# Kernel tuning notes

Measured on AMD Instinct MI355X. Metric: run time of the kernel, lower is better.

The kernel has to match this reference:

```python
import jax, jax.numpy as jnp
import numpy as np

NEG_SLOPE = 0.2

def gat_conv(x_s, x_d, src, dst, W_s, W_d, a_s, a_d, bias, n_dst):
    # PyG GATConv, heads=1, bipartite (-1,-1) input
    hs = x_s @ W_s                          # [Ns, H]
    hd = x_d @ W_d                          # [Nd, H]
    e = jnp.take(hs @ a_s, src) + jnp.take(hd @ a_d, dst)   # [E]
    e = jax.nn.leaky_relu(e, NEG_SLOPE)
    emax = jax.ops.segment_max(e, dst, num_segments=n_dst)
    emax = jax.lax.stop_gradient(jnp.where(jnp.isfinite(emax), emax, 0.0))
    w = jnp.exp(e - emax[dst])              # [E]
    den = jax.ops.segment_sum(w, dst, num_segments=n_dst)   # [Nd]
    msg = jax.ops.segment_sum(w[:, None] * hs[src], dst, num_segments=n_dst)  # [Nd, H]
    return msg / jnp.maximum(den, 1e-16)[:, None] + bias

def setup_inputs() -> dict:
    key = jax.random.key(0)
    ks = jax.random.split(key, 16)
    Na, Nw, D, H, E = 50000, 100000, 128, 128, 640000
    s = 1.0 / np.sqrt(D)
    return {
        "x_artist": jax.random.normal(ks[0], (Na, D), jnp.float32),
        "x_artwork": jax.random.normal(ks[1], (Nw, D), jnp.float32),
        "src_ca": jax.random.randint(ks[2], (E,), 0, Na, jnp.int32),
        "dst_ca": jax.random.randint(ks[3], (E,), 0, Nw, jnp.int32),
        "src_ac": jax.random.randint(ks[4], (E,), 0, Nw, jnp.int32),
        "dst_ac": jax.random.randint(ks[5], (E,), 0, Na, jnp.int32),
        "src_ww": jax.random.randint(ks[6], (E,), 0, Nw, jnp.int32),
        "dst_ww": jax.random.randint(ks[7], (E,), 0, Nw, jnp.int32),
        "Ws": jax.random.normal(ks[8], (3, D, H), jnp.float32) * s,
        "Wd": jax.random.normal(ks[9], (3, D, H), jnp.float32) * s,
        "a_s": jax.random.normal(ks[10], (3, H), jnp.float32) * s,
        "a_d": jax.random.normal(ks[11], (3, H), jnp.float32) * s,
        "b": jax.random.normal(ks[12], (3, H), jnp.float32) * 0.01,
    }

def reference(x_artist, x_artwork, src_ca, dst_ca, src_ac, dst_ac, src_ww, dst_ww, Ws, Wd, a_s, a_d, b):
    Na, Nw = x_artist.shape[0], x_artwork.shape[0]
    # edge type 0: artist->artwork (creates); 1: artwork->artist; 2: artwork->artwork
    out_aw = gat_conv(x_artist, x_artwork, src_ca, dst_ca, Ws[0], Wd[0], a_s[0], a_d[0], b[0], Nw)
    out_aw = out_aw + gat_conv(x_artwork, x_artwork, src_ww, dst_ww, Ws[2], Wd[2], a_s[2], a_d[2], b[2], Nw)  # HeteroConv aggr='sum'
    out_ar = gat_conv(x_artwork, x_artist, src_ac, dst_ac, Ws[1], Wd[1], a_s[1], a_d[1], b[1], Na)
    out_ar = jax.nn.relu(out_ar)
    out_aw = jax.nn.relu(out_aw)
    # concat node-type outputs: [Na+Nw, H]
    return jnp.concatenate([out_ar, out_aw], axis=0)
```

## Files before the change

kernel.cpp:

```cpp
#include <hip/hip_runtime.h>
#include <hip/hip_bf16.h>

#define HD 128
#define NEG_SLOPE 0.2f

typedef __attribute__((ext_vector_type(8))) short short8;
typedef __attribute__((ext_vector_type(4))) float f32x4;

__device__ __forceinline__ float lrelu(float x) {
    return x > 0.f ? x : NEG_SLOPE * x;
}
__device__ __forceinline__ ushort f2bf(float f) {
    __hip_bfloat16 h = __float2bfloat16(f);
    return *(ushort*)&h;
}
__device__ __forceinline__ float bflo(unsigned u) { return __uint_as_float(u << 16); }
__device__ __forceinline__ float bfhi(unsigned u) { return __uint_as_float(u & 0xffff0000u); }

__global__ void k_prep(const float* __restrict__ Ws, const float* __restrict__ Wd,
                       const float* __restrict__ a_s, const float* __restrict__ a_d,
                       ushort* __restrict__ Wt, ushort* __restrict__ vfA,
                       ushort* __restrict__ vfW, int* __restrict__ counts, int nTot) {
    int t = blockIdx.x * blockDim.x + threadIdx.x;
    if (t < nTot) counts[t] = 0;
    if (t < 768) {
        int c = t >> 8;
        int sd = (t >> 7) & 1;
        int d = t & (HD - 1);
        const float* W = sd ? Wd : Ws;
        const float* a = sd ? a_d : a_s;
        const float* Wrow = W + ((size_t)c * HD + d) * HD;
        const float* av = a + c * HD;
        float s = 0.f;
        for (int h = 0; h < HD; h++) s += Wrow[h] * av[h];
        ushort bs = f2bf(s);
        if (c == 0 && sd == 0)      vfA[0 * HD + d] = bs;
        else if (c == 1 && sd == 1) vfA[1 * HD + d] = bs;
        else if (c == 0 && sd == 1) vfW[0 * HD + d] = bs;
        else if (c == 1 && sd == 0) vfW[1 * HD + d] = bs;
        else if (c == 2 && sd == 0) vfW[2 * HD + d] = bs;
        else                        vfW[3 * HD + d] = bs;
    }
    int z = t - 768;
    if (z >= 0 && z < 14 * HD) vfA[2 * HD + z] = 0;
    int z2 = t - 768 - 14 * HD;
    if (z2 >= 0 && z2 < 12 * HD) vfW[4 * HD + z2] = 0;
    int u = t - 768 - 14 * HD - 12 * HD;
    if (u >= 0 && u < 3 * HD * HD) {
        int c = u >> 14;
        int r = u & 16383;
        int n = r >> 7, k = r & 127;
        Wt[u] = f2bf(Ws[((size_t)c << 14) + k * HD + n]);
    }
}

template<int NV>
__device__ __forceinline__ void gemm_body(int blk, const float* __restrict__ X,
        const ushort* __restrict__ Wt, const ushort* __restrict__ vfrag,
        ushort* __restrict__ H16,
        float* __restrict__ a0, float* __restrict__ a1,
        float* __restrict__ a2, float* __restrict__ a3, int nrows) {
    int tid = threadIdx.x;
    int lane = tid & 63;
    int wv = tid >> 6;
    int m = lane & 15;
    int kb = lane >> 4;
    long long row0 = (long long)blk * 64 + wv * 16;
    long long ar = row0 + m;
    if (ar >= nrows) ar = nrows - 1;
    const float* aptr = X + ar * HD + kb * 8;
    const ushort* bptr = Wt + (size_t)m * HD + kb * 8;

    f32x4 acc[8];
    #pragma unroll
    for (int t = 0; t < 8; t++) acc[t] = (f32x4){0.f, 0.f, 0.f, 0.f};
    f32x4 aacc = (f32x4){0.f, 0.f, 0.f, 0.f};

    #pragma unroll
    for (int ks = 0; ks < 4; ks++) {
        float4 A0 = *(const float4*)(aptr + ks * 32);
        float4 A1 = *(const float4*)(aptr + ks * 32 + 4);
        short8 af;
        af[0] = (short)f2bf(A0.x); af[1] = (short)f2bf(A0.y);
        af[2] = (short)f2bf(A0.z); af[3] = (short)f2bf(A0.w);
        af[4] = (short)f2bf(A1.x); af[5] = (short)f2bf(A1.y);
        af[6] = (short)f2bf(A1.z); af[7] = (short)f2bf(A1.w);
        #pragma unroll
        for (int t = 0; t < 8; t++) {
            short8 bf = *(const short8*)(bptr + (size_t)t * 16 * HD + ks * 32);
            acc[t] = __builtin_amdgcn_mfma_f32_16x16x32_bf16(af, bf, acc[t], 0, 0, 0);
        }
        if (NV > 0) {
            short8 vf = *(const short8*)(vfrag + (size_t)m * HD + kb * 8 + ks * 32);
            aacc = __builtin_amdgcn_mfma_f32_16x16x32_bf16(af, vf, aacc, 0, 0, 0);
        }
    }
    int rb = kb * 4;
    #pragma unroll
    for (int t = 0; t < 8; t++) {
        #pragma unroll
        for (int j = 0; j < 4; j++) {
            long long r = row0 + rb + j;
            if (r < nrows) H16[r * HD + t * 16 + m] = f2bf(acc[t][j]);
        }
    }
    if (NV > 0 && m < NV) {
        float* ao = (m == 0) ? a0 : (m == 1) ? a1 : (m == 2) ? a2 : a3;
        #pragma unroll
        for (int j = 0; j < 4; j++) {
            long long r = row0 + rb + j;
            if (r < nrows) ao[r] = aacc[j];
        }
    }
}

__global__ __launch_bounds__(256) void k_hist_gemm(
        const int* __restrict__ d0, const int* __restrict__ d1, const int* __restrict__ d2,
        int* __restrict__ counts, ushort* __restrict__ rank16, int E, int off1, int off2,
        const float* __restrict__ xa, int Na, const ushort* __restrict__ Wt0,
        const ushort* __restrict__ vfA, ushort* __restrict__ hs0,
        float* __restrict__ as0, float* __restrict__ ad1, int g0B,
        const float* __restrict__ xw, int Nw, const ushort* __restrict__ Wt2,
        const ushort* __restrict__ vfW, ushort* __restrict__ hs2,
        float* __restrict__ ad0, float* __restrict__ as1,
        float* __restrict__ as2, float* __restrict__ ad2,
        int ngemm, int total) {
    int b = blockIdx.x;
    int g0 = (int)(((long long)b * ngemm) / total);
    int g1 = (int)(((long long)(b + 1) * ngemm) / total);
    if (g1 > g0) {
        if (g0 < g0B)
            gemm_body<2>(g0, xa, Wt0, vfA, hs0, as0, ad1, nullptr, nullptr, Na);
        else
            gemm_body<4>(g0 - g0B, xw, Wt2, vfW, hs2, ad0, as1, as2, ad2, Nw);
    } else {
        int hb = b - g0;
        int t = hb * 256 + threadIdx.x;
        if (t >= 3 * E) return;
        int gd;
        if (t < E)           gd = d0[t];
        else if (t < 2 * E)  gd = off1 + d1[t - E];
        else                 gd = off2 + d2[t - 2 * E];
        rank16[t] = (ushort)atomicAdd(&counts[gd], 1);
    }
}

__global__ __launch_bounds__(256) void k_gemm1(const float* __restrict__ X,
        const ushort* __restrict__ Wt, ushort* __restrict__ H16, int nrows) {
    gemm_body<0>(blockIdx.x, X, Wt, nullptr, H16, nullptr, nullptr, nullptr, nullptr, nrows);
}

__global__ void k_chunksum(const int* __restrict__ counts, int* __restrict__ chunkSum, int n) {
    __shared__ int sh[256];
    int i = blockIdx.x * 256 + threadIdx.x;
    sh[threadIdx.x] = (i < n) ? counts[i] : 0;
    __syncthreads();
    for (int off = 128; off; off >>= 1) {
        if (threadIdx.x < off) sh[threadIdx.x] += sh[threadIdx.x + off];
        __syncthreads();
    }
    if (threadIdx.x == 0) chunkSum[blockIdx.x] = sh[0];
}

__global__ void k_scanchunk(const int* __restrict__ chunkSum, int* __restrict__ chunkOff, int nChunk) {
    __shared__ int sh[1024];
    int t = threadIdx.x;
    int v = (t < nChunk) ? chunkSum[t] : 0;
    sh[t] = v;
    __syncthreads();
    for (int off = 1; off < 1024; off <<= 1) {
        int add = (t >= off) ? sh[t - off] : 0;
        __syncthreads();
        sh[t] += add;
        __syncthreads();
    }
    if (t < nChunk) chunkOff[t] = sh[t] - v;
}

__global__ void k_rowstart(const int* __restrict__ counts, const int* __restrict__ chunkOff,
                           int* __restrict__ rowStart, int n) {
    __shared__ int sh[256];
    int i = blockIdx.x * 256 + threadIdx.x;
    int t = threadIdx.x;
    int v = (i < n) ? counts[i] : 0;
    sh[t] = v;
    __syncthreads();
    for (int off = 1; off < 256; off <<= 1) {
        int add = (t >= off) ? sh[t - off] : 0;
        __syncthreads();
        sh[t] += add;
        __syncthreads();
    }
    if (i < n) rowStart[i] = chunkOff[blockIdx.x] + sh[t] - v;
}

__global__ void k_fill3(const int* __restrict__ s0, const int* __restrict__ d0,
                        const int* __restrict__ s1, const int* __restrict__ d1,
                        const int* __restrict__ s2, const int* __restrict__ d2,
                        const float* __restrict__ as0, const float* __restrict__ as1,
                        const float* __restrict__ as2,
                        const int* __restrict__ rowStart, const ushort* __restrict__ rank16,
                        int2* __restrict__ ePair, int E, int off1, int off2) {
    int t = blockIdx.x * blockDim.x + threadIdx.x;
    if (t >= 3 * E) return;
    int sv, gd;
    const float* A;
    if (t < E)          { sv = s0[t];        gd = d0[t];        A = as0; }
    else if (t < 2 * E) { int e = t - E;     sv = s1[e]; gd = off1 + d1[e]; A = as1; }
    else                { int e = t - 2 * E; sv = s2[e]; gd = off2 + d2[e]; A = as2; }
    ePair[rowStart[gd] + rank16[t]] = make_int2(sv, __float_as_int(A[sv]));
}

__device__ __forceinline__ void seg_accum(int2 p, int dg, int base, float adv,
                                          const int2* __restrict__ ePair,
                                          const ushort* __restrict__ hs,
                                          int lane, int sub, int fl, float acc[8]) {
    if (dg <= 0) return;
    if (dg <= 64) {
        float av = (lane < dg) ? lrelu(__int_as_float(p.y) + adv) : -1e30f;
        float mm = av;
        #pragma unroll
        for (int off = 32; off; off >>= 1) mm = fmaxf(mm, __shfl_xor(mm, off, 64));
        float w = (lane < dg) ? __expf(av - mm) : 0.f;
        float den = w;
        #pragma unroll
        for (int off = 32; off; off >>= 1) den += __shfl_xor(den, off, 64);
        w *= (1.f / den);
        int s = (lane < dg) ? p.x : 0;
        for (int j0 = 0; j0 < dg; j0 += 4) {
            int idx = j0 + sub;
            float wj = __shfl(w, idx, 64);
            int sj = __shfl(s, idx, 64);
            uint4 u = *(const uint4*)((const unsigned*)hs + ((size_t)sj * HD + fl * 8) / 2);
            acc[0] += wj * bflo(u.x); acc[1] += wj * bfhi(u.x);
            acc[2] += wj * bflo(u.y); acc[3] += wj * bfhi(u.y);
            acc[4] += wj * bflo(u.z); acc[5] += wj * bfhi(u.z);
            acc[6] += wj * bflo(u.w); acc[7] += wj * bfhi(u.w);
        }
    } else {
        float mm = -1e30f;
        for (int i = lane; i < dg; i += 64) {
            int2 q = ePair[base + i];
            mm = fmaxf(mm, lrelu(__int_as_float(q.y) + adv));
        }
        #pragma unroll
        for (int off = 32; off; off >>= 1) mm = fmaxf(mm, __shfl_xor(mm, off, 64));
        float den = 0.f;
        for (int i = lane; i < dg; i += 64) {
            int2 q = ePair[base + i];
            den += __expf(lrelu(__int_as_float(q.y) + adv) - mm);
        }
        #pragma unroll
        for (int off = 32; off; off >>= 1) den += __shfl_xor(den, off, 64);
        float inv = 1.f / den;
        for (int c0 = 0; c0 < dg; c0 += 64) {
            int n = min(64, dg - c0);
            int s = 0; float w = 0.f;
            if (lane < n) {
                int2 q = ePair[base + c0 + lane];
                s = q.x;
                w = __expf(lrelu(__int_as_float(q.y) + adv) - mm) * inv;
            }
            for (int j0 = 0; j0 < n; j0 += 4) {
                int idx = j0 + sub;
                float wj = __shfl(w, idx, 64);
                int sj = __shfl(s, idx, 64);
                uint4 u = *(const uint4*)((const unsigned*)hs + ((size_t)sj * HD + fl * 8) / 2);
                acc[0] += wj * bflo(u.x); acc[1] += wj * bfhi(u.x);
                acc[2] += wj * bflo(u.y); acc[3] += wj * bfhi(u.y);
                acc[4] += wj * bflo(u.z); acc[5] += wj * bfhi(u.z);
                acc[6] += wj * bflo(u.w); acc[7] += wj * bfhi(u.w);
            }
        }
    }
}

__global__ __launch_bounds__(256) void k_agg02(const int2* __restrict__ ePair,
        const int* __restrict__ rowStart, const int* __restrict__ counts,
        const float* __restrict__ ad0_, const float* __restrict__ ad2_,
        const ushort* __restrict__ hs0, const ushort* __restrict__ hs2,
        const float* __restrict__ b0, const float* __restrict__ b2,
        float* __restrict__ out, int Nw, int offR2) {
    int lane = threadIdx.x & 63;
    int d = (int)(((long long)blockIdx.x * blockDim.x + threadIdx.x) >> 6);
    if (d >= Nw) return;
    int sub = lane >> 4, fl = lane & 15;

    int dgA = counts[d],         bA = rowStart[d];
    int dgB = counts[offR2 + d], bB = rowStart[offR2 + d];
    float aA = ad0_[d], aB = ad2_[d];
    int2 pA = make_int2(0, 0), pB = make_int2(0, 0);
    if (dgA > 0 && dgA <= 64 && lane < dgA) pA = ePair[bA + lane];
    if (dgB > 0 && dgB <= 64 && lane < dgB) pB = ePair[bB + lane];

    float acc[8];
    #pragma unroll
    for (int k = 0; k < 8; k++) acc[k] = 0.f;
    seg_accum(pA, dgA, bA, aA, ePair, hs0, lane, sub, fl, acc);
    seg_accum(pB, dgB, bB, aB, ePair, hs2, lane, sub, fl, acc);

    #pragma unroll
    for (int k = 0; k < 8; k++) {
        acc[k] += __shfl_xor(acc[k], 16, 64);
        acc[k] += __shfl_xor(acc[k], 32, 64);
    }
    if (lane < 16) {
        float* orow = out + (size_t)d * HD + fl * 8;
        float vals[8];
        #pragma unroll
        for (int k = 0; k < 8; k++)
            vals[k] = fmaxf(b0[fl * 8 + k] + b2[fl * 8 + k] + acc[k], 0.f);
        *(float4*)&orow[0] = make_float4(vals[0], vals[1], vals[2], vals[3]);
        *(float4*)&orow[4] = make_float4(vals[4], vals[5], vals[6], vals[7]);
    }
}

__global__ __launch_bounds__(256) void k_agg1(const int2* __restrict__ ePair,
        const int* __restrict__ rowStart, const int* __restrict__ counts,
        const float* __restrict__ ad_, const ushort* __restrict__ hs,
        const float* __restrict__ bias, float* __restrict__ out, int Nd) {
    int lane = threadIdx.x & 63;
    int w = (int)(((long long)blockIdx.x * blockDim.x + threadIdx.x) >> 6);
    int d0 = 2 * w, d1 = 2 * w + 1;
    if (d0 >= Nd) return;
    int sub = lane >> 4, fl = lane & 15;

    int dg0 = counts[d0], b0 = rowStart[d0];
    float a0 = ad_[d0];
    int dg1 = 0, b1 = 0; float a1 = 0.f;
    if (d1 < Nd) { dg1 = counts[d1]; b1 = rowStart[d1]; a1 = ad_[d1]; }
    int2 p0 = make_int2(0, 0), p1 = make_int2(0, 0);
    if (dg0 > 0 && dg0 <= 64 && lane < dg0) p0 = ePair[b0 + lane];
    if (dg1 > 0 && dg1 <= 64 && lane < dg1) p1 = ePair[b1 + lane];

    float acc0[8], acc1[8];
    #pragma unroll
    for (int k = 0; k < 8; k++) { acc0[k] = 0.f; acc1[k] = 0.f; }
    seg_accum(p0, dg0, b0, a0, ePair, hs, lane, sub, fl, acc0);
    seg_accum(p1, dg1, b1, a1, ePair, hs, lane, sub, fl, acc1);

    #pragma unroll
    for (int k = 0; k < 8; k++) {
        acc0[k] += __shfl_xor(acc0[k], 16, 64);
        acc0[k] += __shfl_xor(acc0[k], 32, 64);
        acc1[k] += __shfl_xor(acc1[k], 16, 64);
        acc1[k] += __shfl_xor(acc1[k], 32, 64);
    }
    if (lane < 16) {
        float* orow = out + (size_t)d0 * HD + fl * 8;
        float vals[8];
        #pragma unroll
        for (int k = 0; k < 8; k++)
            vals[k] = fmaxf(bias[fl * 8 + k] + acc0[k], 0.f);
        *(float4*)&orow[0] = make_float4(vals[0], vals[1], vals[2], vals[3]);
        *(float4*)&orow[4] = make_float4(vals[4], vals[5], vals[6], vals[7]);
        if (d1 < Nd) {
            float* orow1 = out + (size_t)d1 * HD + fl * 8;
            #pragma unroll
            for (int k = 0; k < 8; k++)
                vals[k] = fmaxf(bias[fl * 8 + k] + acc1[k], 0.f);
            *(float4*)&orow1[0] = make_float4(vals[0], vals[1], vals[2], vals[3]);
            *(float4*)&orow1[4] = make_float4(vals[4], vals[5], vals[6], vals[7]);
        }
    }
}

extern "C" void kernel_launch(void* const* d_in, const int* in_sizes, int n_in,
                              void* d_out, int out_size, void* d_ws, size_t ws_size,
                              hipStream_t stream) {
    const float* x_artist  = (const float*)d_in[0];
    const float* x_artwork = (const float*)d_in[1];
    const int* srcA[3] = {(const int*)d_in[2], (const int*)d_in[4], (const int*)d_in[6]};
    const int* dstA[3] = {(const int*)d_in[3], (const int*)d_in[5], (const int*)d_in[7]};
    const float* Ws  = (const float*)d_in[8];
    const float* Wd  = (const float*)d_in[9];
    const float* a_s = (const float*)d_in[10];
    const float* a_d = (const float*)d_in[11];
    const float* b   = (const float*)d_in[12];
    float* out = (float*)d_out;

    const int Na = in_sizes[0] / HD;
    const int Nw = in_sizes[1] / HD;
    const int E  = in_sizes[2];
    const int nTot = Nw + Na + Nw;
    const int nChunk = (nTot + 255) / 256;

    float* ws = (float*)d_ws;
    size_t off = 0;
    float* as0 = ws + off;  off += Na;
    float* ad1 = ws + off;  off += Na;
    float* ad0 = ws + off;  off += Nw;
    float* as1 = ws + off;  off += Nw;
    float* as2 = ws + off;  off += Nw;
    float* ad2 = ws + off;  off += Nw;
    int* counts   = (int*)(ws + off); off += nTot;
    int* chunkSum = (int*)(ws + off); off += 1024;
    int* chunkOff = (int*)(ws + off); off += 1024;
    int* rowStart = (int*)(ws + off); off += nTot;
    int2* ePair   = (int2*)(ws + off); off += (size_t)2 * 3 * E;
    ushort* rank16 = (ushort*)(ws + off); off += ((size_t)3 * E + 1) / 2;
    ushort* Wt    = (ushort*)(ws + off); off += (3 * HD * HD) / 2;
    ushort* vfA   = (ushort*)(ws + off); off += (16 * HD) / 2;
    ushort* vfW   = (ushort*)(ws + off); off += (16 * HD) / 2;
    ushort* hs0   = (ushort*)(ws + off); off += (size_t)Na * HD / 2;
    ushort* hs2   = (ushort*)(ws + off); off += (size_t)Nw * HD / 2;
    if (ws_size < off * sizeof(float) || nChunk > 1024) return;

    const int off1 = Nw, off2 = Nw + Na;
    const int B = 256;

    k_prep<<<(nTot + B - 1) / B, B, 0, stream>>>(Ws, Wd, a_s, a_d, Wt, vfA, vfW, counts, nTot);

    const int histB = (3 * E + B - 1) / B;
    const int g0B = (Na + 63) / 64;
    const int g2B = (Nw + 63) / 64;
    const int ngemm = g0B + g2B;
    const int total = histB + ngemm;
    k_hist_gemm<<<total, B, 0, stream>>>(dstA[0], dstA[1], dstA[2], counts, rank16,
                                         E, off1, off2,
                                         x_artist, Na, Wt + 0 * HD * HD, vfA, hs0,
                                         as0, ad1, g0B,
                                         x_artwork, Nw, Wt + 2 * HD * HD, vfW, hs2,
                                         ad0, as1, as2, ad2,
                                         ngemm, total);

    k_chunksum<<<nChunk, B, 0, stream>>>(counts, chunkSum, nTot);
    k_scanchunk<<<1, 1024, 0, stream>>>(chunkSum, chunkOff, nChunk);
    k_rowstart<<<nChunk, B, 0, stream>>>(counts, chunkOff, rowStart, nTot);

    k_fill3<<<(3 * E + B - 1) / B, B, 0, stream>>>(srcA[0], dstA[0], srcA[1], dstA[1],
                                                   srcA[2], dstA[2], as0, as1, as2,
                                                   rowStart, rank16, ePair, E, off1, off2);

    k_agg02<<<(Nw + 3) / 4, B, 0, stream>>>(ePair, rowStart, counts, ad0, ad2,
                                            hs0, hs2, b, b + 2 * HD,
                                            out + (size_t)Na * HD, Nw, off2);
    k_gemm1<<<(Nw + 63) / 64, B, 0, stream>>>(x_artwork, Wt + 1 * HD * HD, hs2, Nw);
    int nw1 = (Na + 1) / 2;
    k_agg1<<<(nw1 + 3) / 4, B, 0, stream>>>(ePair, rowStart + off1, counts + off1,
                                            ad1, hs2, b + HD, out, Na);
}
```

Measured before the change: 282.7 us.

## Split hist/GEMM fusion, compute both artwork projections in one pass, pipeline gathers

Splits the combined histogram+GEMM kernel into separate histogram and GEMM kernels. When workspace allows, a new kernel computes the artwork projections for edge types 1 and 2 in a single pass over x_artwork, writing into separate buffers, so the later standalone gemm1 launch is skipped. The small-degree gather loop is also software-pipelined so the next row load is issued before the current one is accumulated. This costs extra workspace memory and removes the overlap the fused hist/GEMM launch gave between atomics and GEMM work.

```diff
diff --git a/kernel.cpp b/kernel.cpp
--- a/kernel.cpp
+++ b/kernel.cpp
@@ -60,9 +60,8 @@
         ushort* __restrict__ H16,
         float* __restrict__ a0, float* __restrict__ a1,
         float* __restrict__ a2, float* __restrict__ a3, int nrows) {
-    int tid = threadIdx.x;
-    int lane = tid & 63;
-    int wv = tid >> 6;
+    int lane = threadIdx.x & 63;
+    int wv = threadIdx.x >> 6;
     int m = lane & 15;
     int kb = lane >> 4;
     long long row0 = (long long)blk * 64 + wv * 16;
@@ -114,40 +113,101 @@
     }
 }
 
-__global__ __launch_bounds__(256) void k_hist_gemm(
-        const int* __restrict__ d0, const int* __restrict__ d1, const int* __restrict__ d2,
-        int* __restrict__ counts, ushort* __restrict__ rank16, int E, int off1, int off2,
-        const float* __restrict__ xa, int Na, const ushort* __restrict__ Wt0,
-        const ushort* __restrict__ vfA, ushort* __restrict__ hs0,
-        float* __restrict__ as0, float* __restrict__ ad1, int g0B,
-        const float* __restrict__ xw, int Nw, const ushort* __restrict__ Wt2,
-        const ushort* __restrict__ vfW, ushort* __restrict__ hs2,
-        float* __restrict__ ad0, float* __restrict__ as1,
-        float* __restrict__ as2, float* __restrict__ ad2,
-        int ngemm, int total) {
-    int b = blockIdx.x;
-    int g0 = (int)(((long long)b * ngemm) / total);
-    int g1 = (int)(((long long)(b + 1) * ngemm) / total);
-    if (g1 > g0) {
-        if (g0 < g0B)
-            gemm_body<2>(g0, xa, Wt0, vfA, hs0, as0, ad1, nullptr, nullptr, Na);
-        else
-            gemm_body<4>(g0 - g0B, xw, Wt2, vfW, hs2, ad0, as1, as2, ad2, Nw);
-    } else {
-        int hb = b - g0;
-        int t = hb * 256 + threadIdx.x;
-        if (t >= 3 * E) return;
-        int gd;
-        if (t < E)           gd = d0[t];
-        else if (t < 2 * E)  gd = off1 + d1[t - E];
-        else                 gd = off2 + d2[t - 2 * E];
-        rank16[t] = (ushort)atomicAdd(&counts[gd], 1);
-    }
-}
-
-__global__ __launch_bounds__(256) void k_gemm1(const float* __restrict__ X,
+__global__ __launch_bounds__(256) void k_gemm0(const float* __restrict__ X,
+        const ushort* __restrict__ Wt, const ushort* __restrict__ vfA,
+        ushort* __restrict__ H16, float* __restrict__ as0, float* __restrict__ ad1, int nrows) {
+    gemm_body<2>(blockIdx.x, X, Wt, vfA, H16, as0, ad1, nullptr, nullptr, nrows);
+}
+__global__ __launch_bounds__(256) void k_gemm2f(const float* __restrict__ X,
+        const ushort* __restrict__ Wt, const ushort* __restrict__ vfW,
+        ushort* __restrict__ H16, float* __restrict__ ad0, float* __restrict__ as1,
+        float* __restrict__ as2, float* __restrict__ ad2, int nrows) {
+    gemm_body<4>(blockIdx.x, X, Wt, vfW, H16, ad0, as1, as2, ad2, nrows);
+}
+__global__ __launch_bounds__(256) void k_gemm1f(const float* __restrict__ X,
         const ushort* __restrict__ Wt, ushort* __restrict__ H16, int nrows) {
     gemm_body<0>(blockIdx.x, X, Wt, nullptr, H16, nullptr, nullptr, nullptr, nullptr, nrows);
+}
+
+__global__ __launch_bounds__(256) void k_gemmW(const float* __restrict__ X,
+        const ushort* __restrict__ WtA, const ushort* __restrict__ WtB,
+        const ushort* __restrict__ vf, ushort* __restrict__ hsA, ushort* __restrict__ hsB,
+        float* __restrict__ a0, float* __restrict__ a1,
+        float* __restrict__ a2, float* __restrict__ a3, int nrows) {
+    int lane = threadIdx.x & 63;
+    int wv = threadIdx.x >> 6;
+    int m = lane & 15;
+    int kb = lane >> 4;
+    long long row0 = (long long)blockIdx.x * 64 + wv * 16;
+    long long ar = row0 + m;
+    if (ar >= nrows) ar = nrows - 1;
+    const float* aptr = X + ar * HD + kb * 8;
+    const ushort* bA = WtA + (size_t)m * HD + kb * 8;
+    const ushort* bB = WtB + (size_t)m * HD + kb * 8;
+    int rb = kb * 4;
+
+    #pragma unroll
+    for (int half = 0; half < 2; half++) {
+        f32x4 accA[4], accB[4];
+        #pragma unroll
+        for (int t = 0; t < 4; t++) {
+            accA[t] = (f32x4){0.f, 0.f, 0.f, 0.f};
+            accB[t] = (f32x4){0.f, 0.f, 0.f, 0.f};
+        }
+        f32x4 aacc = (f32x4){0.f, 0.f, 0.f, 0.f};
+        #pragma unroll
+        for (int ks = 0; ks < 4; ks++) {
+            float4 A0 = *(const float4*)(aptr + ks * 32);
+            float4 A1 = *(const float4*)(aptr + ks * 32 + 4);
+            short8 af;
+            af[0] = (short)f2bf(A0.x); af[1] = (short)f2bf(A0.y);
+            af[2] = (short)f2bf(A0.z); af[3] = (short)f2bf(A0.w);
+            af[4] = (short)f2bf(A1.x); af[5] = (short)f2bf(A1.y);
+            af[6] = (short)f2bf(A1.z); af[7] = (short)f2bf(A1.w);
+            #pragma unroll
+            for (int t = 0; t < 4; t++) {
+                short8 bfA = *(const short8*)(bA + (size_t)(half * 4 + t) * 16 * HD + ks * 32);
+                accA[t] = __builtin_amdgcn_mfma_f32_16x16x32_bf16(af, bfA, accA[t], 0, 0, 0);
+                short8 bfB = *(const short8*)(bB + (size_t)(half * 4 + t) * 16 * HD + ks * 32);
+                accB[t] = __builtin_amdgcn_mfma_f32_16x16x32_bf16(af, bfB, accB[t], 0, 0, 0);
+            }
+            if (half == 0) {
+                short8 vfr = *(const short8*)(vf + (size_t)m * HD + kb * 8 + ks * 32);
+                aacc = __builtin_amdgcn_mfma_f32_16x16x32_bf16(af, vfr, aacc, 0, 0, 0);
+            }
+        }
+        #pragma unroll
+        for (int t = 0; t < 4; t++) {
+            #pragma unroll
+            for (int j = 0; j < 4; j++) {
+                long long r = row0 + rb + j;
+                if (r < nrows) {
+                    hsA[r * HD + (half * 4 + t) * 16 + m] = f2bf(accA[t][j]);
+                    hsB[r * HD + (half * 4 + t) * 16 + m] = f2bf(accB[t][j]);
+                }
+            }
+        }
+        if (half == 0 && m < 4) {
+            float* ao = (m == 0) ? a0 : (m == 1) ? a1 : (m == 2) ? a2 : a3;
+            #pragma unroll
+            for (int j = 0; j < 4; j++) {
+                long long r = row0 + rb + j;
+                if (r < nrows) ao[r] = aacc[j];
+            }
+        }
+    }
+}
+
+__global__ void k_hist3(const int* __restrict__ d0, const int* __restrict__ d1,
+                        const int* __restrict__ d2, int* __restrict__ counts,
+                        ushort* __restrict__ rank16, int E, int off1, int off2) {
+    int t = blockIdx.x * blockDim.x + threadIdx.x;
+    if (t >= 3 * E) return;
+    int gd;
+    if (t < E)           gd = d0[t];
+    else if (t < 2 * E)  gd = off1 + d1[t - E];
+    else                 gd = off2 + d2[t - 2 * E];
+    rank16[t] = (ushort)atomicAdd(&counts[gd], 1);
 }
 
 __global__ void k_chunksum(const int* __restrict__ counts, int* __restrict__ chunkSum, int n) {
@@ -211,6 +271,30 @@
     ePair[rowStart[gd] + rank16[t]] = make_int2(sv, __float_as_int(A[sv]));
 }
 
+__device__ __forceinline__ void acc8(uint4 u, float wj, float acc[8]) {
+    acc[0] += wj * bflo(u.x); acc[1] += wj * bfhi(u.x);
+    acc[2] += wj * bflo(u.y); acc[3] += wj * bfhi(u.y);
+    acc[4] += wj * bflo(u.z); acc[5] += wj * bfhi(u.z);
+    acc[6] += wj * bflo(u.w); acc[7] += wj * bfhi(u.w);
+}
+
+__device__ __forceinline__ void seg_gather_pipe(int s, float w, int dg,
+        const ushort* __restrict__ hs, int sub, int fl, float acc[8]) {
+    if (dg <= 0) return;
+    const unsigned* hp = (const unsigned*)hs + fl * 4;
+    float wj = __shfl(w, sub, 64);
+    int sj = __shfl(s, sub, 64);
+    uint4 u = *(const uint4*)(hp + (size_t)sj * (HD / 2));
+    for (int j0 = 4; j0 < dg; j0 += 4) {
+        float wn = __shfl(w, j0 + sub, 64);
+        int sn = __shfl(s, j0 + sub, 64);
+        uint4 un = *(const uint4*)(hp + (size_t)sn * (HD / 2));
+        acc8(u, wj, acc);
+        wj = wn; u = un;
+    }
+    acc8(u, wj, acc);
+}
+
 __device__ __forceinline__ void seg_accum(int2 p, int dg, int base, float adv,
                                           const int2* __restrict__ ePair,
                                           const ushort* __restrict__ hs,
@@ -227,16 +311,7 @@
         for (int off = 32; off; off >>= 1) den += __shfl_xor(den, off, 64);
         w *= (1.f / den);
         int s = (lane < dg) ? p.x : 0;
-        for (int j0 = 0; j0 < dg; j0 += 4) {
-            int idx = j0 + sub;
-            float wj = __shfl(w, idx, 64);
-            int sj = __shfl(s, idx, 64);
-            uint4 u = *(const uint4*)((const unsigned*)hs + ((size_t)sj * HD + fl * 8) / 2);
-            acc[0] += wj * bflo(u.x); acc[1] += wj * bfhi(u.x);
-            acc[2] += wj * bflo(u.y); acc[3] += wj * bfhi(u.y);
-            acc[4] += wj * bflo(u.z); acc[5] += wj * bfhi(u.z);
-            acc[6] += wj * bflo(u.w); acc[7] += wj * bfhi(u.w);
-        }
+        seg_gather_pipe(s, w, dg, hs, sub, fl, acc);
     } else {
         float mm = -1e30f;
         for (int i = lane; i < dg; i += 64) {
@@ -266,10 +341,7 @@
                 float wj = __shfl(w, idx, 64);
                 int sj = __shfl(s, idx, 64);
                 uint4 u = *(const uint4*)((const unsigned*)hs + ((size_t)sj * HD + fl * 8) / 2);
-                acc[0] += wj * bflo(u.x); acc[1] += wj * bfhi(u.x);
-                acc[2] += wj * bflo(u.y); acc[3] += wj * bfhi(u.y);
-                acc[4] += wj * bflo(u.z); acc[5] += wj * bfhi(u.z);
-                acc[6] += wj * bflo(u.w); acc[7] += wj * bfhi(u.w);
+                acc8(u, wj, acc);
             }
         }
     }
@@ -406,28 +478,33 @@
     ushort* hs2   = (ushort*)(ws + off); off += (size_t)Nw * HD / 2;
     if (ws_size < off * sizeof(float) || nChunk > 1024) return;
 
+    size_t offBig = off + (size_t)Nw * HD / 2;
+    bool bigWS = (ws_size >= offBig * sizeof(float));
+    ushort* hs1 = bigWS ? (ushort*)(ws + off) : hs2;
+
     const int off1 = Nw, off2 = Nw + Na;
     const int B = 256;
 
     k_prep<<<(nTot + B - 1) / B, B, 0, stream>>>(Ws, Wd, a_s, a_d, Wt, vfA, vfW, counts, nTot);
 
-    const int histB = (3 * E + B - 1) / B;
-    const int g0B = (Na + 63) / 64;
-    const int g2B = (Nw + 63) / 64;
-    const int ngemm = g0B + g2B;
-    const int total = histB + ngemm;
-    k_hist_gemm<<<total, B, 0, stream>>>(dstA[0], dstA[1], dstA[2], counts, rank16,
-                                         E, off1, off2,
-                                         x_artist, Na, Wt + 0 * HD * HD, vfA, hs0,
-                                         as0, ad1, g0B,
-                                         x_artwork, Nw, Wt + 2 * HD * HD, vfW, hs2,
-                                         ad0, as1, as2, ad2,
-                                         ngemm, total);
+    k_hist3<<<(3 * E + B - 1) / B, B, 0, stream>>>(dstA[0], dstA[1], dstA[2], counts,
+                                                   rank16, E, off1, off2);
 
     k_chunksum<<<nChunk, B, 0, stream>>>(counts, chunkSum, nTot);
     k_scanchunk<<<1, 1024, 0, stream>>>(chunkSum, chunkOff, nChunk);
     k_rowstart<<<nChunk, B, 0, stream>>>(counts, chunkOff, rowStart, nTot);
 
+    k_gemm0<<<(Na + 63) / 64, B, 0, stream>>>(x_artist, Wt + 0 * HD * HD, vfA,
+                                              hs0, as0, ad1, Na);
+    if (bigWS) {
+        k_gemmW<<<(Nw + 63) / 64, B, 0, stream>>>(x_artwork, Wt + 1 * HD * HD,
+                                                  Wt + 2 * HD * HD, vfW, hs1, hs2,
+                                                  ad0, as1, as2, ad2, Nw);
+    } else {
+        k_gemm2f<<<(Nw + 63) / 64, B, 0, stream>>>(x_artwork, Wt + 2 * HD * HD, vfW,
+                                                   hs2, ad0, as1, as2, ad2, Nw);
+    }
+
     k_fill3<<<(3 * E + B - 1) / B, B, 0, stream>>>(srcA[0], dstA[0], srcA[1], dstA[1],
                                                    srcA[2], dstA[2], as0, as1, as2,
                                                    rowStart, rank16, ePair, E, off1, off2);
@@ -435,8 +512,9 @@
     k_agg02<<<(Nw + 3) / 4, B, 0, stream>>>(ePair, rowStart, counts, ad0, ad2,
                                             hs0, hs2, b, b + 2 * HD,
                                             out + (size_t)Na * HD, Nw, off2);
-    k_gemm1<<<(Nw + 63) / 64, B, 0, stream>>>(x_artwork, Wt + 1 * HD * HD, hs2, Nw);
+    if (!bigWS)
+        k_gemm1f<<<(Nw + 63) / 64, B, 0, stream>>>(x_artwork, Wt + 1 * HD * HD, hs2, Nw);
     int nw1 = (Na + 1) / 2;
     k_agg1<<<(nw1 + 3) / 4, B, 0, stream>>>(ePair, rowStart + off1, counts + off1,
-                                            ad1, hs2, b + HD, out, Na);
-}
+                                            ad1, hs1, b + HD, out, Na);
+}
```

Result: slower. 334.8 us (+18.4%).

## Split hist/gemm kernels, merge scan stages, add separate hs1 buffer, pipeline gathers

Applied to the files above, without the earlier changes.

Separates the fused histogram+GEMM kernel into a standalone histogram kernel and a GEMM kernel. The chunk-offset scan is folded into the row-start kernel, with each block summing preceding chunk sums itself, which removes one launch. When workspace allows, the third projection gets its own buffer and is computed before aggregation instead of overwriting hs2 between the two aggregation kernels. The small-degree gather loop is software-pipelined so the next row load is issued before the current one is accumulated. The trade-off is the loss of the overlap between histogram and GEMM work that the fused kernel provided, plus a redundant prefix sum in every row-start block.

```diff
diff --git a/kernel.cpp b/kernel.cpp
--- a/kernel.cpp
+++ b/kernel.cpp
@@ -60,9 +60,8 @@
         ushort* __restrict__ H16,
         float* __restrict__ a0, float* __restrict__ a1,
         float* __restrict__ a2, float* __restrict__ a3, int nrows) {
-    int tid = threadIdx.x;
-    int lane = tid & 63;
-    int wv = tid >> 6;
+    int lane = threadIdx.x & 63;
+    int wv = threadIdx.x >> 6;
     int m = lane & 15;
     int kb = lane >> 4;
     long long row0 = (long long)blk * 64 + wv * 16;
@@ -114,40 +113,36 @@
     }
 }
 
-__global__ __launch_bounds__(256) void k_hist_gemm(
-        const int* __restrict__ d0, const int* __restrict__ d1, const int* __restrict__ d2,
-        int* __restrict__ counts, ushort* __restrict__ rank16, int E, int off1, int off2,
-        const float* __restrict__ xa, int Na, const ushort* __restrict__ Wt0,
+__global__ __launch_bounds__(256) void k_gemm02(
+        const float* __restrict__ xa, const ushort* __restrict__ Wt0,
         const ushort* __restrict__ vfA, ushort* __restrict__ hs0,
-        float* __restrict__ as0, float* __restrict__ ad1, int g0B,
-        const float* __restrict__ xw, int Nw, const ushort* __restrict__ Wt2,
+        float* __restrict__ as0, float* __restrict__ ad1, int Na, int g0B,
+        const float* __restrict__ xw, const ushort* __restrict__ Wt2,
         const ushort* __restrict__ vfW, ushort* __restrict__ hs2,
         float* __restrict__ ad0, float* __restrict__ as1,
-        float* __restrict__ as2, float* __restrict__ ad2,
-        int ngemm, int total) {
+        float* __restrict__ as2, float* __restrict__ ad2, int Nw) {
     int b = blockIdx.x;
-    int g0 = (int)(((long long)b * ngemm) / total);
-    int g1 = (int)(((long long)(b + 1) * ngemm) / total);
-    if (g1 > g0) {
-        if (g0 < g0B)
-            gemm_body<2>(g0, xa, Wt0, vfA, hs0, as0, ad1, nullptr, nullptr, Na);
-        else
-            gemm_body<4>(g0 - g0B, xw, Wt2, vfW, hs2, ad0, as1, as2, ad2, Nw);
-    } else {
-        int hb = b - g0;
-        int t = hb * 256 + threadIdx.x;
-        if (t >= 3 * E) return;
-        int gd;
-        if (t < E)           gd = d0[t];
-        else if (t < 2 * E)  gd = off1 + d1[t - E];
-        else                 gd = off2 + d2[t - 2 * E];
-        rank16[t] = (ushort)atomicAdd(&counts[gd], 1);
-    }
-}
-
-__global__ __launch_bounds__(256) void k_gemm1(const float* __restrict__ X,
+    if (b < g0B)
+        gemm_body<2>(b, xa, Wt0, vfA, hs0, as0, ad1, nullptr, nullptr, Na);
+    else
+        gemm_body<4>(b - g0B, xw, Wt2, vfW, hs2, ad0, as1, as2, ad2, Nw);
+}
+
+__global__ __launch_bounds__(256) void k_gemm1f(const float* __restrict__ X,
         const ushort* __restrict__ Wt, ushort* __restrict__ H16, int nrows) {
     gemm_body<0>(blockIdx.x, X, Wt, nullptr, H16, nullptr, nullptr, nullptr, nullptr, nrows);
+}
+
+__global__ void k_hist3(const int* __restrict__ d0, const int* __restrict__ d1,
+                        const int* __restrict__ d2, int* __restrict__ counts,
+                        ushort* __restrict__ rank16, int E, int off1, int off2) {
+    int t = blockIdx.x * blockDim.x + threadIdx.x;
+    if (t >= 3 * E) return;
+    int gd;
+    if (t < E)           gd = d0[t];
+    else if (t < 2 * E)  gd = off1 + d1[t - E];
+    else                 gd = off2 + d2[t - 2 * E];
+    rank16[t] = (ushort)atomicAdd(&counts[gd], 1);
 }
 
 __global__ void k_chunksum(const int* __restrict__ counts, int* __restrict__ chunkSum, int n) {
@@ -162,26 +157,23 @@
     if (threadIdx.x == 0) chunkSum[blockIdx.x] = sh[0];
 }
 
-__global__ void k_scanchunk(const int* __restrict__ chunkSum, int* __restrict__ chunkOff, int nChunk) {
-    __shared__ int sh[1024];
+__global__ void k_rowstart2(const int* __restrict__ counts, const int* __restrict__ chunkSum,
+                            int* __restrict__ rowStart, int n) {
+    __shared__ int sh[256];
+    __shared__ int chunkOffS;
+    int bid = blockIdx.x;
     int t = threadIdx.x;
-    int v = (t < nChunk) ? chunkSum[t] : 0;
-    sh[t] = v;
+    int psum = 0;
+    for (int i = t; i < bid; i += 256) psum += chunkSum[i];
+    sh[t] = psum;
     __syncthreads();
-    for (int off = 1; off < 1024; off <<= 1) {
-        int add = (t >= off) ? sh[t - off] : 0;
+    for (int off = 128; off; off >>= 1) {
+        if (t < off) sh[t] += sh[t + off];
         __syncthreads();
-        sh[t] += add;
-        __syncthreads();
-    }
-    if (t < nChunk) chunkOff[t] = sh[t] - v;
-}
-
-__global__ void k_rowstart(const int* __restrict__ counts, const int* __restrict__ chunkOff,
-                           int* __restrict__ rowStart, int n) {
-    __shared__ int sh[256];
-    int i = blockIdx.x * 256 + threadIdx.x;
-    int t = threadIdx.x;
+    }
+    if (t == 0) chunkOffS = sh[0];
+    __syncthreads();
+    int i = bid * 256 + t;
     int v = (i < n) ? counts[i] : 0;
     sh[t] = v;
     __syncthreads();
@@ -191,7 +183,7 @@
         sh[t] += add;
         __syncthreads();
     }
-    if (i < n) rowStart[i] = chunkOff[blockIdx.x] + sh[t] - v;
+    if (i < n) rowStart[i] = chunkOffS + sh[t] - v;
 }
 
 __global__ void k_fill3(const int* __restrict__ s0, const int* __restrict__ d0,
@@ -211,6 +203,30 @@
     ePair[rowStart[gd] + rank16[t]] = make_int2(sv, __float_as_int(A[sv]));
 }
 
+__device__ __forceinline__ void acc8(uint4 u, float wj, float acc[8]) {
+    acc[0] += wj * bflo(u.x); acc[1] += wj * bfhi(u.x);
+    acc[2] += wj * bflo(u.y); acc[3] += wj * bfhi(u.y);
+    acc[4] += wj * bflo(u.z); acc[5] += wj * bfhi(u.z);
+    acc[6] += wj * bflo(u.w); acc[7] += wj * bfhi(u.w);
+}
+
+__device__ __forceinline__ void seg_gather_pipe(int s, float w, int dg,
+        const ushort* __restrict__ hs, int sub, int fl, float acc[8]) {
+    if (dg <= 0) return;
+    const unsigned* hp = (const unsigned*)hs + fl * 4;
+    float wj = __shfl(w, sub, 64);
+    int sj = __shfl(s, sub, 64);
+    uint4 u = *(const uint4*)(hp + (size_t)sj * (HD / 2));
+    for (int j0 = 4; j0 < dg; j0 += 4) {
+        float wn = __shfl(w, j0 + sub, 64);
+        int sn = __shfl(s, j0 + sub, 64);
+        uint4 un = *(const uint4*)(hp + (size_t)sn * (HD / 2));
+        acc8(u, wj, acc);
+        wj = wn; u = un;
+    }
+    acc8(u, wj, acc);
+}
+
 __device__ __forceinline__ void seg_accum(int2 p, int dg, int base, float adv,
                                           const int2* __restrict__ ePair,
                                           const ushort* __restrict__ hs,
@@ -227,16 +243,7 @@
         for (int off = 32; off; off >>= 1) den += __shfl_xor(den, off, 64);
         w *= (1.f / den);
         int s = (lane < dg) ? p.x : 0;
-        for (int j0 = 0; j0 < dg; j0 += 4) {
-            int idx = j0 + sub;
-            float wj = __shfl(w, idx, 64);
-            int sj = __shfl(s, idx, 64);
-            uint4 u = *(const uint4*)((const unsigned*)hs + ((size_t)sj * HD + fl * 8) / 2);
-            acc[0] += wj * bflo(u.x); acc[1] += wj * bfhi(u.x);
-            acc[2] += wj * bflo(u.y); acc[3] += wj * bfhi(u.y);
-            acc[4] += wj * bflo(u.z); acc[5] += wj * bfhi(u.z);
-            acc[6] += wj * bflo(u.w); acc[7] += wj * bfhi(u.w);
-        }
+        seg_gather_pipe(s, w, dg, hs, sub, fl, acc);
     } else {
         float mm = -1e30f;
         for (int i = lane; i < dg; i += 64) {
@@ -266,10 +273,7 @@
                 float wj = __shfl(w, idx, 64);
                 int sj = __shfl(s, idx, 64);
                 uint4 u = *(const uint4*)((const unsigned*)hs + ((size_t)sj * HD + fl * 8) / 2);
-                acc[0] += wj * bflo(u.x); acc[1] += wj * bfhi(u.x);
-                acc[2] += wj * bflo(u.y); acc[3] += wj * bfhi(u.y);
-                acc[4] += wj * bflo(u.z); acc[5] += wj * bfhi(u.z);
-                acc[6] += wj * bflo(u.w); acc[7] += wj * bfhi(u.w);
+                acc8(u, wj, acc);
             }
         }
     }
@@ -394,8 +398,7 @@
     float* as2 = ws + off;  off += Nw;
     float* ad2 = ws + off;  off += Nw;
     int* counts   = (int*)(ws + off); off += nTot;
-    int* chunkSum = (int*)(ws + off); off += 1024;
-    int* chunkOff = (int*)(ws + off); off += 1024;
+    int* chunkSum = (int*)(ws + off); off += nChunk;
     int* rowStart = (int*)(ws + off); off += nTot;
     int2* ePair   = (int2*)(ws + off); off += (size_t)2 * 3 * E;
     ushort* rank16 = (ushort*)(ws + off); off += ((size_t)3 * E + 1) / 2;
@@ -404,29 +407,31 @@
     ushort* vfW   = (ushort*)(ws + off); off += (16 * HD) / 2;
     ushort* hs0   = (ushort*)(ws + off); off += (size_t)Na * HD / 2;
     ushort* hs2   = (ushort*)(ws + off); off += (size_t)Nw * HD / 2;
-    if (ws_size < off * sizeof(float) || nChunk > 1024) return;
+    if (ws_size < off * sizeof(float)) return;
+
+    size_t offBig = off + (size_t)Nw * HD / 2;
+    bool bigWS = (ws_size >= offBig * sizeof(float));
+    ushort* hs1 = bigWS ? (ushort*)(ws + off) : hs2;
 
     const int off1 = Nw, off2 = Nw + Na;
     const int B = 256;
 
     k_prep<<<(nTot + B - 1) / B, B, 0, stream>>>(Ws, Wd, a_s, a_d, Wt, vfA, vfW, counts, nTot);
 
-    const int histB = (3 * E + B - 1) / B;
+    k_hist3<<<(3 * E + B - 1) / B, B, 0, stream>>>(dstA[0], dstA[1], dstA[2], counts,
+                                                   rank16, E, off1, off2);
+
+    k_chunksum<<<nChunk, B, 0, stream>>>(counts, chunkSum, nTot);
+    k_rowstart2<<<nChunk, B, 0, stream>>>(counts, chunkSum, rowStart, nTot);
+
     const int g0B = (Na + 63) / 64;
     const int g2B = (Nw + 63) / 64;
-    const int ngemm = g0B + g2B;
-    const int total = histB + ngemm;
-    k_hist_gemm<<<total, B, 0, stream>>>(dstA[0], dstA[1], dstA[2], counts, rank16,
-                                         E, off1, off2,
-                                         x_artist, Na, Wt + 0 * HD * HD, vfA, hs0,
-                                         as0, ad1, g0B,
-                                         x_artwork, Nw, Wt + 2 * HD * HD, vfW, hs2,
-                                         ad0, as1, as2, ad2,
-                                         ngemm, total);
-
-    k_chunksum<<<nChunk, B, 0, stream>>>(counts, chunkSum, nTot);
-    k_scanchunk<<<1, 1024, 0, stream>>>(chunkSum, chunkOff, nChunk);
-    k_rowstart<<<nChunk, B, 0, stream>>>(counts, chunkOff, rowStart, nTot);
+    k_gemm02<<<g0B + g2B, B, 0, stream>>>(x_artist, Wt + 0 * HD * HD, vfA, hs0,
+                                          as0, ad1, Na, g0B,
+                                          x_artwork, Wt + 2 * HD * HD, vfW, hs2,
+                                          ad0, as1, as2, ad2, Nw);
+    if (bigWS)
+        k_gemm1f<<<g2B, B, 0, stream>>>(x_artwork, Wt + 1 * HD * HD, hs1, Nw);
 
     k_fill3<<<(3 * E + B - 1) / B, B, 0, stream>>>(srcA[0], dstA[0], srcA[1], dstA[1],
                                                    srcA[2], dstA[2], as0, as1, as2,
@@ -435,8 +440,9 @@
     k_agg02<<<(Nw + 3) / 4, B, 0, stream>>>(ePair, rowStart, counts, ad0, ad2,
                                             hs0, hs2, b, b + 2 * HD,
                                             out + (size_t)Na * HD, Nw, off2);
-    k_gemm1<<<(Nw + 63) / 64, B, 0, stream>>>(x_artwork, Wt + 1 * HD * HD, hs2, Nw);
+    if (!bigWS)
+        k_gemm1f<<<g2B, B, 0, stream>>>(x_artwork, Wt + 1 * HD * HD, hs1, Nw);
     int nw1 = (Na + 1) / 2;
     k_agg1<<<(nw1 + 3) / 4, B, 0, stream>>>(ePair, rowStart + off1, counts + off1,
-                                            ad1, hs2, b + HD, out, Na);
-}
+                                            ad1, hs1, b + HD, out, Na);
+}
```

New measurement: 344.8 us. 22.0% more time.
